# Kernel tuning notes

Measured on AMD Instinct MI355X. Metric: run time of the kernel, lower is better.

## Reference

```python
import jax, jax.numpy as jnp
import numpy as np

B, N, D, R, W, H, I = 256, 2048, 128, 4, 1, 1024, 1024
CI = I + R * D                       # controller input size (1536)
IF = 2 * D * W + 2 * W + 1 + 4 * R + D * R   # interface size (787)
OPI = H + R * D                      # output_proj input (1536)


def _norm(v):
    # F.normalize(dim=-1): x / max(||x||, eps)
    return v / jnp.maximum(jnp.linalg.norm(v, axis=-1, keepdims=True), 1e-12)


def setup_inputs() -> dict:
    key = jax.random.key(0)
    ks = jax.random.split(key, 16)
    u = lambda k, shape, fan: jax.random.uniform(k, shape, jnp.float32, -1.0 / np.sqrt(fan), 1.0 / np.sqrt(fan))
    return {
        "x": jax.random.normal(ks[0], (B, I), jnp.float32),
        "memory": jax.random.normal(ks[1], (N, D), jnp.float32) * np.sqrt(2.0 / (N + D)),  # xavier-ish
        "usage": jax.random.uniform(ks[2], (N,), jnp.float32),          # usage in [0,1)
        "link": jax.random.normal(ks[3], (N, N), jnp.float32) * 0.01,   # non-trivial link state
        "W_ih": u(ks[4], (4 * H, CI), H),
        "W_hh": u(ks[5], (4 * H, H), H),
        "b_ih": u(ks[6], (4 * H,), H),
        "b_hh": u(ks[7], (4 * H,), H),
        "W_if": u(ks[8], (IF, H), H),
        "b_if": u(ks[9], (IF,), H),
        "W_out": u(ks[10], (H, OPI), OPI),
        "b_out": u(ks[11], (H,), OPI),
    }


def reference(x, memory, usage, link, W_ih, W_hh, b_ih, b_hh, W_if, b_if, W_out, b_out):
    # initial uniform read weights (prev state at first step)
    prev_rw = jnp.full((B, R, N), 1.0 / N, x.dtype)
    read_flat = (prev_rw @ memory).reshape(B, -1)                 # (B, R*D)
    cin = jnp.concatenate([x, read_flat], axis=-1)                # (B, CI)

    # single LSTM step, h0 = c0 = 0, torch gate order i,f,g,o
    g = cin @ W_ih.T + b_ih + b_hh
    gi, gf, gg, go = jnp.split(g, 4, axis=-1)
    c = jax.nn.sigmoid(gi) * jnp.tanh(gg)
    h = jax.nn.sigmoid(go) * jnp.tanh(c)                          # (B, H) controller out

    itf = h @ W_if.T + b_if                                       # (B, IF)
    o = 0
    write_vals = itf[:, o:o + D * W].reshape(B, W, D); o += D * W
    erase = jax.nn.sigmoid(itf[:, o:o + D * W]).reshape(B, W, D); o += D * W
    write_gates = jax.nn.sigmoid(itf[:, o:o + W]); o += W         # (B, W)
    alloc_gate = jax.nn.sigmoid(itf[:, o:o + 1]); o += 1          # (B, 1)
    o += W                                                        # free gates (parsed, unused)
    read_modes = jax.nn.softmax(itf[:, o:o + 3 * R].reshape(B, R, 3), -1); o += 3 * R
    read_str = jax.nn.softplus(itf[:, o:o + R]); o += R           # (B, R)
    read_keys = itf[:, o:o + D * R].reshape(B, R, D)

    # content addressing for the write (strength = 1)
    mem_n = _norm(memory)
    cw = jax.nn.softmax(_norm(write_vals.mean(1)) @ mem_n.T, -1)  # (B, N)

    # allocation weighting: sorted-usage cumprod (per source semantics)
    idx = jnp.argsort(usage)
    su = usage[idx]
    cp = jnp.cumprod(1.0 - su)
    alloc_s = jnp.concatenate([su[:1], su[1:] * cp[:-1]])
    alloc = jnp.zeros_like(usage).at[idx].set(alloc_s)[None, :] * alloc_gate  # (B, N)

    write_w = write_gates[:, :, None] * (0.5 * cw + 0.5 * alloc)[:, None, :]  # (B, W, N)

    # temporal link update: batch-mean of diag-masked outer product, decay 0.9
    lu = jnp.einsum('bwn,bwm->nm', write_w, write_w) / B
    lu = lu * (1.0 - jnp.eye(N, dtype=lu.dtype))
    link_new = link * 0.9 + lu * 0.1

    # memory write (erase then add, batch-mean)
    ev = erase * write_gates[:, :, None]
    av = write_vals * write_gates[:, :, None]
    erase_mat = jnp.einsum('bwn,bwd->nd', write_w, ev) / B
    add_mat = jnp.einsum('bwn,bwd->nd', write_w, av) / B
    mem_new = memory * (1.0 - erase_mat) + add_mat

    # read addressing on updated memory and updated link (all R heads vectorized)
    sim = jnp.einsum('brd,nd->brn', _norm(read_keys), _norm(mem_new))
    content_r = jax.nn.softmax(sim * read_str[:, :, None], -1)    # (B, R, N)
    backward_w = jnp.einsum('brn,nm->brm', prev_rw, link_new)     # mode 1: prev @ L
    forward_w = jnp.einsum('brn,mn->brm', prev_rw, link_new)      # mode 2: prev @ L^T
    new_rw = (read_modes[..., 0:1] * content_r
              + read_modes[..., 1:2] * backward_w
              + read_modes[..., 2:3] * forward_w)                 # (B, R, N)

    read_out = (new_rw @ mem_new).reshape(B, -1)                  # (B, R*D)
    out = jnp.concatenate([h, read_out], axis=-1) @ W_out.T + b_out
    return out
```

## Files before the change

kernel.cpp:

```cpp
#include <hip/hip_runtime.h>
#include <cmath>

#define DEVI __device__ __forceinline__

DEVI float sigm(float x){ return 1.f/(1.f+expf(-x)); }

typedef __attribute__((ext_vector_type(8))) _Float16 half8;
typedef __attribute__((ext_vector_type(4))) _Float16 half4;
typedef __attribute__((ext_vector_type(4))) float float4v;


__global__ void k_zero(float* __restrict__ p, int n){
  int i = blockIdx.x*256 + threadIdx.x;
  if (i < n) p[i] = 0.f;
}

__global__ __launch_bounds__(256) void k_stage1(
    const float* __restrict__ mem, float* __restrict__ cm, _Float16* __restrict__ mem_h,
    const float* __restrict__ usage, float* __restrict__ alloc,
    const float* __restrict__ link, float* __restrict__ rsl, float* __restrict__ cslp)
{
  __shared__ float smem[4][132];
  const int blk = blockIdx.x, t = threadIdx.x;
  const int wv = t >> 6, lane = t & 63;

  if (blk < 128){
    int rbase = blk*16 + wv*4;
    float x0[4], x1[4], ss[4];
    #pragma unroll
    for (int u = 0; u < 4; u++){
      const float* a = mem + (size_t)(rbase+u)*128;
      x0[u] = a[lane]; x1[u] = a[lane+64];
    }
    #pragma unroll
    for (int u = 0; u < 4; u++) ss[u] = x0[u]*x0[u] + x1[u]*x1[u];
    #pragma unroll
    for (int o = 1; o < 64; o <<= 1){
      #pragma unroll
      for (int u = 0; u < 4; u++) ss[u] += __shfl_xor(ss[u], o);
    }
    float c0 = 0.f, c1 = 0.f;
    #pragma unroll
    for (int u = 0; u < 4; u++){
      float invn = 1.f / fmaxf(sqrtf(ss[u]), 1e-12f);
      mem_h[(size_t)(rbase+u)*128 + lane]      = (_Float16)(x0[u]*invn);
      mem_h[(size_t)(rbase+u)*128 + 64 + lane] = (_Float16)(x1[u]*invn);
      c0 += x0[u]; c1 += x1[u];
    }
    smem[wv][lane] = c0; smem[wv][64+lane] = c1;
    __syncthreads();
    if (t < 128) atomicAdd(&cm[t], smem[0][t]+smem[1][t]+smem[2][t]+smem[3][t]);
  } else if (blk < 384){
    int pb = blk - 128;
    int r0 = pb*8;
    int c0 = t*8;
    float4v v0[8], v1[8];
    #pragma unroll
    for (int u = 0; u < 8; u++){
      const float* lp = link + (size_t)(r0+u)*2048 + c0;
      v0[u] = *(const float4v*)lp;
      v1[u] = *(const float4v*)(lp+4);
    }
    float colacc[8];
    #pragma unroll
    for (int j = 0; j < 8; j++) colacc[j] = 0.f;
    float rowpart[8];
    #pragma unroll
    for (int u = 0; u < 8; u++){
      float s = 0.f;
      #pragma unroll
      for (int j = 0; j < 4; j++){
        colacc[j]   += v0[u][j]; colacc[4+j] += v1[u][j];
        s += v0[u][j] + v1[u][j];
      }
      rowpart[u] = s;
    }
    #pragma unroll
    for (int o = 1; o < 64; o <<= 1){
      #pragma unroll
      for (int u = 0; u < 8; u++) rowpart[u] += __shfl_xor(rowpart[u], o);
    }
    if (lane == 0){
      #pragma unroll
      for (int u = 0; u < 8; u++) smem[wv][u] = rowpart[u];
    }
    __syncthreads();
    if (t < 8) rsl[r0+t] = smem[0][t]+smem[1][t]+smem[2][t]+smem[3][t];
    float4v w0, w1;
    #pragma unroll
    for (int j = 0; j < 4; j++){ w0[j] = colacc[j]; w1[j] = colacc[4+j]; }
    *(float4v*)&cslp[(size_t)pb*2048 + c0]     = w0;
    *(float4v*)&cslp[(size_t)pb*2048 + c0 + 4] = w1;
  } else {
    int n = (blk - 384)*4 + wv;
    float un = usage[n];
    float prod = 1.f;
    #pragma unroll
    for (int i = 0; i < 32; i++){
      int m = lane + i*64;
      float um = usage[m];
      bool before = (um < un) || (um == un && m < n);
      prod *= before ? (1.f - um) : 1.f;
    }
    #pragma unroll
    for (int o = 32; o > 0; o >>= 1) prod *= __shfl_xor(prod, o);
    if (lane == 0) alloc[n] = un * prod;
  }
}

__global__ __launch_bounds__(256) void k_cin_csl(const float* __restrict__ x,
    const float* __restrict__ cm, _Float16* __restrict__ cin,
    const float* __restrict__ cslp, float* __restrict__ csl)
{
  __shared__ float sm[4][64];
  int blk = blockIdx.x, t = threadIdx.x;
  if (blk < 1536){
    int idx = blk*256 + t;
    int b = idx / 1536, k = idx - b*1536;
    float v = (k < 1024) ? x[b*1024 + k] : cm[(k-1024) & 127] * (1.f/2048.f);
    cin[idx] = (_Float16)v;
  } else {
    int j = blk - 1536;
    int tl = t & 63, q = t >> 6;
    int col = j*64 + tl;
    float s = 0.f;
    for (int p = q*64; p < q*64 + 64; p += 4){
      s += cslp[(size_t)(p+0)*2048 + col] + cslp[(size_t)(p+1)*2048 + col]
         + cslp[(size_t)(p+2)*2048 + col] + cslp[(size_t)(p+3)*2048 + col];
    }
    sm[q][tl] = s;
    __syncthreads();
    if (q == 0) csl[col] = sm[0][tl]+sm[1][tl]+sm[2][tl]+sm[3][tl];
  }
}

__global__ void k_lstm(const float* __restrict__ g, _Float16* __restrict__ h){
  int idx = blockIdx.x*256 + threadIdx.x;
  int b = idx >> 10, j = idx & 1023;
  const float* gr = g + (size_t)b*4096;
  float c = sigm(gr[j]) * tanhf(gr[2048 + j]);
  h[idx] = (_Float16)(sigm(gr[3072 + j]) * tanhf(c));
}

#define QA 264
#define QB 520

template<typename TB> struct BReg;
template<> struct BReg<_Float16>{
  half8 v;
  DEVI void load(const _Float16* p){ v = *(const half8*)p; }
  DEVI half8 get() const { return v; }
};
template<> struct BReg<float>{
  float4v a, b;
  DEVI void load(const float* p){ a = *(const float4v*)p; b = *(const float4v*)(p+4); }
  DEVI half8 get() const {
    half8 h;
    #pragma unroll
    for (int j = 0; j < 4; j++){ h[j] = (_Float16)a[j]; h[4+j] = (_Float16)b[j]; }
    return h;
  }
};

template<typename TB>
__global__ __launch_bounds__(256) void gemm_t(
    const _Float16* __restrict__ A, const TB* __restrict__ Bm, float* __restrict__ C,
    int M, int N, int K,
    const float* __restrict__ bias1, const float* __restrict__ bias2)
{
  __shared__ _Float16 Ah[2][8*QA];
  __shared__ _Float16 Bh[2][8*QB];
  const int tid = threadIdx.x;
  const int m0 = blockIdx.y*32, n0 = blockIdx.x*64;
  const int T = K >> 6;
  const int arow = tid >> 3, aq = tid & 7;
  const int brow = tid >> 3, bq = tid & 7;
  int nB0 = n0 + brow;      if (nB0 >= N) nB0 = N - 1;
  int nB1 = n0 + brow + 32; if (nB1 >= N) nB1 = N - 1;
  const _Float16* Aptr = A + (size_t)(m0 + arow)*K + aq*8;
  const TB* Bp0 = Bm + (size_t)nB0*K + bq*8;
  const TB* Bp1 = Bm + (size_t)nB1*K + bq*8;
  const int wA  = aq*QA + arow*8;
  const int wB0 = bq*QB + brow*8;
  const int wB1 = bq*QB + (brow+32)*8;
  const int wv_ = tid >> 6, lane = tid & 63;
  const int fq = lane >> 4, fr = lane & 15;
  const int m16 = (wv_ & 1)*16, nb = (wv_ >> 1)*32;

  half8 ra;
  BReg<TB> rb0, rb1;
  ra = *(const half8*)(Aptr);
  rb0.load(Bp0);
  rb1.load(Bp1);
  *(half8*)&Ah[0][wA]  = ra;
  *(half8*)&Bh[0][wB0] = rb0.get();
  *(half8*)&Bh[0][wB1] = rb1.get();
  __syncthreads();

  float4v acc0 = {0.f,0.f,0.f,0.f}, acc1 = {0.f,0.f,0.f,0.f};
  for (int t = 0; t < T; t++){
    const int cur = t & 1, nxt = cur ^ 1;
    if (t+1 < T){
      ra = *(const half8*)(Aptr + (t+1)*64);
      rb0.load(Bp0 + (t+1)*64);
      rb1.load(Bp1 + (t+1)*64);
    }
    #pragma unroll
    for (int s = 0; s < 2; s++){
      int q = s*4 + fq;
      half8 a  = *(half8*)&Ah[cur][q*QA + (m16+fr)*8];
      half8 b0 = *(half8*)&Bh[cur][q*QB + (nb+fr)*8];
      half8 b1 = *(half8*)&Bh[cur][q*QB + (nb+16+fr)*8];
      acc0 = __builtin_amdgcn_mfma_f32_16x16x32_f16(a, b0, acc0, 0, 0, 0);
      acc1 = __builtin_amdgcn_mfma_f32_16x16x32_f16(a, b1, acc1, 0, 0, 0);
    }
    if (t+1 < T){
      *(half8*)&Ah[nxt][wA]  = ra;
      *(half8*)&Bh[nxt][wB0] = rb0.get();
      *(half8*)&Bh[nxt][wB1] = rb1.get();
    }
    __syncthreads();
  }

  const int colA = n0 + nb + fr, colB = colA + 16;
  #pragma unroll
  for (int i = 0; i < 4; i++){
    int m = m0 + m16 + fq*4 + i;
    if (colA < N){
      float v = acc0[i];
      if (bias1) v += bias1[colA];
      if (bias2) v += bias2[colA];
      C[(size_t)m*N + colA] = v;
    }
    if (colB < N){
      float v = acc1[i];
      if (bias1) v += bias1[colB];
      if (bias2) v += bias2[colB];
      C[(size_t)m*N + colB] = v;
    }
  }
}

DEVI float blockReduce128(float v, float* lds2){
  #pragma unroll
  for (int o = 32; o > 0; o >>= 1) v += __shfl_xor(v, o);
  int w = threadIdx.x >> 6;
  __syncthreads();
  if ((threadIdx.x & 63) == 0) lds2[w] = v;
  __syncthreads();
  return lds2[0] + lds2[1];
}

__global__ __launch_bounds__(128) void k_parse(const float* __restrict__ itf,
    _Float16* __restrict__ wv_h, float* __restrict__ ev, float* __restrict__ av,
    float* __restrict__ wg_, float* __restrict__ ag_,
    float* __restrict__ rm0, float* __restrict__ rm1, float* __restrict__ rm2,
    _Float16* __restrict__ rks_h)
{
  __shared__ float red[2];
  int b = blockIdx.x, t = threadIdx.x;
  const float* it = itf + (size_t)b*787;
  float wg = sigm(it[256]);
  float ag = sigm(it[257]);
  if (t == 0){ wg_[b] = wg; ag_[b] = ag; }
  float w = it[t];
  av[b*128 + t] = w * wg;
  ev[b*128 + t] = sigm(it[128 + t]) * wg;
  float ss = blockReduce128(w*w, red);
  float invwv = 1.f / fmaxf(sqrtf(ss), 1e-12f);
  wv_h[b*128 + t] = (_Float16)(w * invwv);
  if (t < 4){
    int rr = t;
    float m0v = it[259 + rr*3 + 0], m1v = it[259 + rr*3 + 1], m2v = it[259 + rr*3 + 2];
    float mx = fmaxf(m0v, fmaxf(m1v, m2v));
    float e0 = expf(m0v - mx), e1 = expf(m1v - mx), e2 = expf(m2v - mx);
    float inv = 1.f / (e0 + e1 + e2);
    rm0[b*4 + rr] = e0*inv; rm1[b*4 + rr] = e1*inv; rm2[b*4 + rr] = e2*inv;
  }
  #pragma unroll
  for (int rr = 0; rr < 4; rr++){
    float kv = it[275 + rr*128 + t];
    float ks = blockReduce128(kv*kv, red);
    float sx = it[271 + rr];
    float str = fmaxf(sx, 0.f) + log1pf(expf(-fabsf(sx)));
    float invk = 1.f / fmaxf(sqrtf(ks), 1e-12f);
    rks_h[((size_t)b*4 + rr)*128 + t] = (_Float16)(kv * invk * str);
  }
}

__global__ __launch_bounds__(256) void k_softmax_ww(float* __restrict__ P,
    const float* __restrict__ alloc, const float* __restrict__ wg, const float* __restrict__ ag){
  __shared__ float red[4];
  float* p = P + (size_t)blockIdx.x*2048;
  int t = threadIdx.x;
  float r[8];
  float mx = -3.4e38f;
  #pragma unroll
  for (int i = 0; i < 8; i++){ r[i] = p[t + i*256]; mx = fmaxf(mx, r[i]); }
  #pragma unroll
  for (int o = 32; o > 0; o >>= 1) mx = fmaxf(mx, __shfl_xor(mx, o));
  if ((t & 63) == 0) red[t >> 6] = mx;
  __syncthreads();
  mx = fmaxf(fmaxf(red[0], red[1]), fmaxf(red[2], red[3]));
  float s = 0.f;
  #pragma unroll
  for (int i = 0; i < 8; i++){ r[i] = expf(r[i] - mx); s += r[i]; }
  #pragma unroll
  for (int o = 32; o > 0; o >>= 1) s += __shfl_xor(s, o);
  __syncthreads();
  if ((t & 63) == 0) red[t >> 6] = s;
  __syncthreads();
  s = red[0] + red[1] + red[2] + red[3];
  float inv = 1.f / s;
  float wgb = wg[blockIdx.x], agb = ag[blockIdx.x];
  #pragma unroll
  for (int i = 0; i < 8; i++){
    int col = t + i*256;
    p[col] = wgb*(0.5f*r[i]*inv + 0.5f*alloc[col]*agb);
  }
}

__global__ __launch_bounds__(256) void k_bwfw(const float* __restrict__ ww,
                       const float* __restrict__ wg, const float* __restrict__ ag,
                       const float* __restrict__ alloc,
                       const float* __restrict__ rowsum, const float* __restrict__ colsum,
                       float* __restrict__ bw, float* __restrict__ fw){
  __shared__ float sq[4][64], sd[4][64];
  __shared__ float sred[4];
  __shared__ float tbs[256];
  int t = threadIdx.x & 63, z = threadIdx.x >> 6;
  int m = blockIdx.x*64 + t;
  float sa = 0.f;
  #pragma unroll
  for (int i = 0; i < 8; i++) sa += alloc[threadIdx.x + i*256];
  #pragma unroll
  for (int o = 32; o > 0; o >>= 1) sa += __shfl_xor(sa, o);
  if (t == 0) sred[z] = sa;
  __syncthreads();
  sa = (sred[0]+sred[1]) + (sred[2]+sred[3]);
  tbs[threadIdx.x] = wg[threadIdx.x]*(0.5f + 0.5f*ag[threadIdx.x]*sa);
  __syncthreads();
  float q = 0.f, dd = 0.f;
  for (int b = z*64; b < z*64 + 64; b += 4){
    float w0 = ww[(size_t)(b+0)*2048 + m];
    float w1 = ww[(size_t)(b+1)*2048 + m];
    float w2 = ww[(size_t)(b+2)*2048 + m];
    float w3 = ww[(size_t)(b+3)*2048 + m];
    q  = fmaf(tbs[b+0], w0, q);  dd = fmaf(w0, w0, dd);
    q  = fmaf(tbs[b+1], w1, q);  dd = fmaf(w1, w1, dd);
    q  = fmaf(tbs[b+2], w2, q);  dd = fmaf(w2, w2, dd);
    q  = fmaf(tbs[b+3], w3, q);  dd = fmaf(w3, w3, dd);
  }
  sq[z][t] = q; sd[z][t] = dd;
  __syncthreads();
  if (z == 0){
    q  = sq[0][t] + sq[1][t] + sq[2][t] + sq[3][t];
    dd = sd[0][t] + sd[1][t] + sd[2][t] + sd[3][t];
    float lus = (q - dd) * (1.f/256.f);
    bw[m] = (0.9f*colsum[m] + 0.1f*lus) * (1.f/2048.f);
    fw[m] = (0.9f*rowsum[m] + 0.1f*lus) * (1.f/2048.f);
  }
}

__global__ __launch_bounds__(256) void k_memupdate_fused(const float* __restrict__ ww,
    const float* __restrict__ ev, const float* __restrict__ av,
    const float* __restrict__ mem, const float* __restrict__ bw, const float* __restrict__ fw,
    _Float16* __restrict__ memn_h, _Float16* __restrict__ memnT_h,
    float* __restrict__ bwm, float* __restrict__ fwm)
{
  __shared__ float Ws[16][34];
  __shared__ float Es[16][132], Vs[16][132];
  __shared__ float lb[128], lf[128];
  __shared__ _Float16 Traw[32][132];
  const int n0 = blockIdx.x*32;
  const int tid = threadIdx.x, tx = tid & 31, ty = tid >> 5;
  if (tid < 128){ lb[tid] = 0.f; lf[tid] = 0.f; }
  const int wk = tid >> 4, wn = (tid & 15)*2;
  const int ek = tid >> 4, ec = (tid & 15)*8;
  float ae[4][4] = {}, aa[4][4] = {};
  for (int k0 = 0; k0 < 256; k0 += 16){
    float2 vw  = *(const float2*)(ww + (size_t)(k0+wk)*2048 + n0 + wn);
    float4 ve0 = *(const float4*)(ev + (size_t)(k0+ek)*128 + ec);
    float4 ve1 = *(const float4*)(ev + (size_t)(k0+ek)*128 + ec + 4);
    float4 va0 = *(const float4*)(av + (size_t)(k0+ek)*128 + ec);
    float4 va1 = *(const float4*)(av + (size_t)(k0+ek)*128 + ec + 4);
    __syncthreads();
    Ws[wk][wn] = vw.x; Ws[wk][wn+1] = vw.y;
    *(float4*)&Es[ek][ec] = ve0; *(float4*)&Es[ek][ec+4] = ve1;
    *(float4*)&Vs[ek][ec] = va0; *(float4*)&Vs[ek][ec+4] = va1;
    __syncthreads();
    #pragma unroll
    for (int k = 0; k < 16; k++){
      float a[4], e[4], v[4];
      #pragma unroll
      for (int i = 0; i < 4; i++) a[i] = Ws[k][ty*4+i];
      #pragma unroll
      for (int j = 0; j < 4; j++){ e[j] = Es[k][tx*4+j]; v[j] = Vs[k][tx*4+j]; }
      #pragma unroll
      for (int i = 0; i < 4; i++)
        #pragma unroll
        for (int j = 0; j < 4; j++){
          ae[i][j] = fmaf(a[i], e[j], ae[i][j]);
          aa[i][j] = fmaf(a[i], v[j], aa[i][j]);
        }
    }
  }
  float ab[4] = {0,0,0,0}, af[4] = {0,0,0,0};
  #pragma unroll
  for (int i = 0; i < 4; i++){
    int n = n0 + ty*4 + i;
    float bwn = bw[n], fwn = fw[n];
    float v[4]; float ss = 0.f;
    #pragma unroll
    for (int j = 0; j < 4; j++){
      int d = tx*4 + j;
      float em = ae[i][j]*(1.f/256.f), am = aa[i][j]*(1.f/256.f);
      float mv = mem[(size_t)n*128 + d]*(1.f - em) + am;
      v[j] = mv; ss += mv*mv;
      ab[j] = fmaf(bwn, mv, ab[j]);
      af[j] = fmaf(fwn, mv, af[j]);
    }
    #pragma unroll
    for (int o = 1; o < 32; o <<= 1) ss += __shfl_xor(ss, o);
    float invn = 1.f / fmaxf(sqrtf(ss), 1e-12f);
    half4 hn, hr;
    #pragma unroll
    for (int j = 0; j < 4; j++){ hn[j] = (_Float16)(v[j]*invn); hr[j] = (_Float16)v[j]; }
    *(half4*)(memn_h + (size_t)n*128 + tx*4) = hn;
    *(half4*)&Traw[ty*4+i][tx*4] = hr;
  }
  __syncthreads();
  {
    int d = tid >> 1, seg = (tid & 1)*16;
    half8 o0, o1;
    #pragma unroll
    for (int j = 0; j < 8; j++){ o0[j] = Traw[seg+j][d]; o1[j] = Traw[seg+8+j][d]; }
    *(half8*)(memnT_h + (size_t)d*2048 + n0 + seg)     = o0;
    *(half8*)(memnT_h + (size_t)d*2048 + n0 + seg + 8) = o1;
  }
  #pragma unroll
  for (int j = 0; j < 4; j++){
    atomicAdd(&lb[tx*4+j], ab[j]);
    atomicAdd(&lf[tx*4+j], af[j]);
  }
  __syncthreads();
  if (tid < 128){
    atomicAdd(&bwm[tid], lb[tid]);
    atomicAdd(&fwm[tid], lf[tid]);
  }
}

__global__ __launch_bounds__(256) void k_flash(
    const _Float16* __restrict__ Q, const _Float16* __restrict__ Kh,
    const _Float16* __restrict__ Vt,
    float* __restrict__ pacc, float* __restrict__ pm, float* __restrict__ pl)
{
  __shared__ _Float16 Pl[4][16][32];
  __shared__ float cmb[4][2080];
  __shared__ float scl[4][16];
  const int tid = threadIdx.x;
  const int qt = blockIdx.x >> 2, kc = blockIdx.x & 3;
  const int wv = tid >> 6, lane = tid & 63;
  const int fq = lane >> 4, fr = lane & 15;
  const int kw0 = kc*512 + wv*128;

  half8 aq[4];
  #pragma unroll
  for (int c = 0; c < 4; c++)
    aq[c] = *(const half8*)(Q + (size_t)(qt*16 + fr)*128 + c*32 + fq*8);

  float m[4] = {-3.0e38f,-3.0e38f,-3.0e38f,-3.0e38f};
  float l[4] = {0.f,0.f,0.f,0.f};
  float4v acc[8] = {};
  for (int s = 0; s < 4; s++){
    const int kb = kw0 + s*32;
    float4v S0 = {0,0,0,0}, S1 = {0,0,0,0};
    #pragma unroll
    for (int c = 0; c < 4; c++){
      half8 b0 = *(const half8*)(Kh + (size_t)(kb + fr)*128      + c*32 + fq*8);
      half8 b1 = *(const half8*)(Kh + (size_t)(kb + 16 + fr)*128 + c*32 + fq*8);
      S0 = __builtin_amdgcn_mfma_f32_16x16x32_f16(aq[c], b0, S0, 0, 0, 0);
      S1 = __builtin_amdgcn_mfma_f32_16x16x32_f16(aq[c], b1, S1, 0, 0, 0);
    }
    float mt[4], ps[4];
    #pragma unroll
    for (int i = 0; i < 4; i++) mt[i] = fmaxf(S0[i], S1[i]);
    #pragma unroll
    for (int o = 1; o < 16; o <<= 1){
      #pragma unroll
      for (int i = 0; i < 4; i++) mt[i] = fmaxf(mt[i], __shfl_xor(mt[i], o));
    }
    #pragma unroll
    for (int i = 0; i < 4; i++){
      float mn = fmaxf(m[i], mt[i]);
      float al = expf(m[i] - mn);
      float p0 = expf(S0[i] - mn), p1 = expf(S1[i] - mn);
      S0[i] = p0; S1[i] = p1;
      ps[i] = p0 + p1;
      l[i] *= al;
      m[i] = mn;
      #pragma unroll
      for (int c = 0; c < 8; c++) acc[c][i] *= al;
    }
    #pragma unroll
    for (int o = 1; o < 16; o <<= 1){
      #pragma unroll
      for (int i = 0; i < 4; i++) ps[i] += __shfl_xor(ps[i], o);
    }
    #pragma unroll
    for (int i = 0; i < 4; i++) l[i] += ps[i];
    #pragma unroll
    for (int i = 0; i < 4; i++){
      Pl[wv][fq*4+i][fr]      = (_Float16)S0[i];
      Pl[wv][fq*4+i][16 + fr] = (_Float16)S1[i];
    }
    half8 pf = *(half8*)&Pl[wv][fr][fq*8];
    #pragma unroll
    for (int c = 0; c < 8; c++){
      half8 bv = *(const half8*)(Vt + (size_t)(c*16 + fr)*2048 + kb + fq*8);
      acc[c] = __builtin_amdgcn_mfma_f32_16x16x32_f16(pf, bv, acc[c], 0, 0, 0);
    }
  }
  if (fr == 0){
    #pragma unroll
    for (int i = 0; i < 4; i++){
      cmb[wv][fq*4+i]      = m[i];
      cmb[wv][16 + fq*4+i] = l[i];
    }
  }
  #pragma unroll
  for (int c = 0; c < 8; c++)
    #pragma unroll
    for (int i = 0; i < 4; i++)
      cmb[wv][32 + (fq*4+i)*128 + c*16 + fr] = acc[c][i];
  __syncthreads();
  if (tid < 16){
    float mm = fmaxf(fmaxf(cmb[0][tid], cmb[1][tid]), fmaxf(cmb[2][tid], cmb[3][tid]));
    float ll = 0.f;
    #pragma unroll
    for (int w = 0; w < 4; w++){
      float e = expf(cmb[w][tid] - mm);
      scl[w][tid] = e;
      ll += e * cmb[w][16 + tid];
    }
    pm[blockIdx.x*16 + tid] = mm;
    pl[blockIdx.x*16 + tid] = ll;
  }
  __syncthreads();
  for (int e = tid; e < 2048; e += 256){
    int q = e >> 7;
    float a = scl[0][q]*cmb[0][32+e] + scl[1][q]*cmb[1][32+e]
            + scl[2][q]*cmb[2][32+e] + scl[3][q]*cmb[3][32+e];
    pacc[(size_t)blockIdx.x*2048 + e] = a;
  }
}

__global__ void k_hro_comb(const _Float16* __restrict__ h, const float* __restrict__ pacc,
                           const float* __restrict__ pm, const float* __restrict__ pl,
                           const float* __restrict__ rm0, const float* __restrict__ rm1,
                           const float* __restrict__ rm2, const float* __restrict__ bwm,
                           const float* __restrict__ fwm, _Float16* __restrict__ hro){
  int idx = blockIdx.x*256 + threadIdx.x;
  int b = idx / 1536, k = idx - b*1536;
  if (k < 1024){
    hro[idx] = h[b*1024 + k];
  } else {
    int r = k - 1024, rh = r >> 7, d = r & 127;
    int row = b*4 + rh, qt = row >> 4, q = row & 15;
    float mm = -3.0e38f;
    #pragma unroll
    for (int kc = 0; kc < 4; kc++) mm = fmaxf(mm, pm[(qt*4+kc)*16 + q]);
    float num = 0.f, den = 0.f;
    #pragma unroll
    for (int kc = 0; kc < 4; kc++){
      float e = expf(pm[(qt*4+kc)*16 + q] - mm);
      den += e * pl[(qt*4+kc)*16 + q];
      num += e * pacc[(size_t)(qt*4+kc)*2048 + q*128 + d];
    }
    float pv = num / den;
    hro[idx] = (_Float16)(rm0[row]*pv + rm1[row]*bwm[d] + rm2[row]*fwm[d]);
  }
}


extern "C" void kernel_launch(void* const* d_in, const int* in_sizes, int n_in,
                              void* d_out, int out_size, void* d_ws, size_t ws_size,
                              hipStream_t stream)
{
  const float* x     = (const float*)d_in[0];
  const float* mem   = (const float*)d_in[1];
  const float* usage = (const float*)d_in[2];
  const float* link  = (const float*)d_in[3];
  const float* W_ih  = (const float*)d_in[4];
  const float* b_ih  = (const float*)d_in[6];
  const float* b_hh  = (const float*)d_in[7];
  const float* W_if  = (const float*)d_in[8];
  const float* b_if  = (const float*)d_in[9];
  const float* W_out = (const float*)d_in[10];
  const float* b_out = (const float*)d_in[11];
  float* out = (float*)d_out;
  float* ws  = (float*)d_ws;

  float* cm     = ws + 0;
  float* csl    = ws + 128;
  float* bwm    = ws + 2176;
  float* fwm    = ws + 2304;
  float* bw     = ws + 2688;
  float* fw     = ws + 4736;
  float* wg     = ws + 6784;
  float* ag     = ws + 7040;
  float* rm0    = ws + 7296;
  float* rm1    = ws + 8320;
  float* rm2    = ws + 9344;
  float* alloc  = ws + 10368;
  float* rsl    = ws + 12416;
  float* ev     = ws + 14464;
  float* av     = ws + 47232;
  float* g      = ws + 80000;
  float* itf    = ws + 1128576;
  float* ww     = ws + 1330048;
  float* pacc   = ws + 1854336;
  float* pm     = ws + 2378624;
  float* pl     = ws + 2382720;
  _Float16* wv_h    = (_Float16*)(ws + 2386816);
  _Float16* mem_h   = (_Float16*)(ws + 2403200);
  _Float16* memn_h  = (_Float16*)(ws + 2534272);
  _Float16* memnT_h = (_Float16*)(ws + 2665344);
  _Float16* rks_h   = (_Float16*)(ws + 2796416);
  _Float16* hro_h   = (_Float16*)(ws + 2861952);
  _Float16* cin_h   = (_Float16*)(ws + 3058560);
  _Float16* h_h     = (_Float16*)(ws + 3255168);
  float* cslp       = ws + 3386240;

  k_zero<<<10, 256, 0, stream>>>(ws, 2432);

  k_stage1<<<896, 256, 0, stream>>>(mem, cm, mem_h, usage, alloc, link, rsl, cslp);
  k_cin_csl<<<1568, 256, 0, stream>>>(x, cm, cin_h, cslp, csl);

  gemm_t<float><<<dim3(64,8), 256, 0, stream>>>(cin_h, W_ih, g, 256, 4096, 1536, b_ih, b_hh);
  k_lstm<<<1024, 256, 0, stream>>>(g, h_h);

  gemm_t<float><<<dim3(13,8), 256, 0, stream>>>(h_h, W_if, itf, 256, 787, 1024, b_if, nullptr);
  k_parse<<<256, 128, 0, stream>>>(itf, wv_h, ev, av, wg, ag, rm0, rm1, rm2, rks_h);

  gemm_t<_Float16><<<dim3(32,8), 256, 0, stream>>>(wv_h, mem_h, ww, 256, 2048, 128, nullptr, nullptr);
  k_softmax_ww<<<256, 256, 0, stream>>>(ww, alloc, wg, ag);

  k_bwfw<<<32, 256, 0, stream>>>(ww, wg, ag, alloc, rsl, csl, bw, fw);

  k_memupdate_fused<<<64, 256, 0, stream>>>(ww, ev, av, mem, bw, fw, memn_h, memnT_h, bwm, fwm);

  k_flash<<<256, 256, 0, stream>>>(rks_h, memn_h, memnT_h, pacc, pm, pl);

  k_hro_comb<<<1536, 256, 0, stream>>>(h_h, pacc, pm, pl, rm0, rm1, rm2, bwm, fwm, hro_h);
  gemm_t<float><<<dim3(16,8), 256, 0, stream>>>(hro_h, W_out, out, 256, 1024, 1536, b_out, nullptr);

  (void)in_sizes; (void)n_in; (void)out_size; (void)ws_size;
}
```

Baseline: 236.3 us.

## Fuse LSTM gates into W_ih GEMM, skip forget gate, fold bwfw into memupdate

A dedicated GEMM kernel computes only the input, cell and output gate columns of W_ih. The forget gate is unused because c0 is zero, so this skips a quarter of that GEMM. The kernel applies the LSTM nonlinearity in its epilogue, which removes the fp32 gate buffer round-trip and the separate k_lstm launch. The k_bwfw reduction over write weights is also folded into k_memupdate_fused, reusing the ww tiles already staged in shared memory and dropping one launch plus the bw/fw global buffers. The trade-off is more registers and LDS in both kernels, and a smaller 32x32 output tile in the LSTM GEMM.

```diff
diff --git a/kernel.cpp b/kernel.cpp
--- a/kernel.cpp
+++ b/kernel.cpp
@@ -134,16 +134,9 @@
   }
 }
 
-__global__ void k_lstm(const float* __restrict__ g, _Float16* __restrict__ h){
-  int idx = blockIdx.x*256 + threadIdx.x;
-  int b = idx >> 10, j = idx & 1023;
-  const float* gr = g + (size_t)b*4096;
-  float c = sigm(gr[j]) * tanhf(gr[2048 + j]);
-  h[idx] = (_Float16)(sigm(gr[3072 + j]) * tanhf(c));
-}
-
 #define QA 264
 #define QB 520
+#define QB3 776
 
 template<typename TB> struct BReg;
 template<> struct BReg<_Float16>{
@@ -238,6 +231,96 @@
       if (bias2) v += bias2[colB];
       C[(size_t)m*N + colB] = v;
     }
+  }
+}
+
+__global__ __launch_bounds__(256) void k_gemm_lstm(
+    const _Float16* __restrict__ A, const float* __restrict__ W,
+    const float* __restrict__ b_ih, const float* __restrict__ b_hh,
+    _Float16* __restrict__ h)
+{
+  __shared__ _Float16 Ah[2][8*QA];
+  __shared__ _Float16 Bh[2][8*QB3];
+  const int tid = threadIdx.x;
+  const int m0 = blockIdx.y*32, c0 = blockIdx.x*32;
+  const int T = 24;
+  const int arow = tid >> 3, aq = tid & 7;
+  const int brow = tid >> 3, bq = tid & 7;
+  const _Float16* Aptr = A + (size_t)(m0 + arow)*1536 + aq*8;
+  const float* Bpi = W + (size_t)(       c0 + brow)*1536 + bq*8;
+  const float* Bpg = W + (size_t)(2048 + c0 + brow)*1536 + bq*8;
+  const float* Bpo = W + (size_t)(3072 + c0 + brow)*1536 + bq*8;
+  const int wA  = aq*QA + arow*8;
+  const int wBi = bq*QB3 + brow*8;
+  const int wBg = bq*QB3 + (32+brow)*8;
+  const int wBo = bq*QB3 + (64+brow)*8;
+  const int wv_ = tid >> 6, lane = tid & 63;
+  const int fq = lane >> 4, fr = lane & 15;
+  const int m16 = (wv_ & 1)*16, c16 = (wv_ >> 1)*16;
+
+  half8 ra0, ra1;
+  BReg<float> ri0, rg0, ro0, ri1, rg1, ro1;
+  ra0 = *(const half8*)(Aptr);
+  ri0.load(Bpi); rg0.load(Bpg); ro0.load(Bpo);
+  ra1 = *(const half8*)(Aptr + 64);
+  ri1.load(Bpi + 64); rg1.load(Bpg + 64); ro1.load(Bpo + 64);
+  *(half8*)&Ah[0][wA]  = ra0;
+  *(half8*)&Bh[0][wBi] = ri0.get();
+  *(half8*)&Bh[0][wBg] = rg0.get();
+  *(half8*)&Bh[0][wBo] = ro0.get();
+  __syncthreads();
+
+  float4v acci = {0.f,0.f,0.f,0.f}, accg = {0.f,0.f,0.f,0.f}, acco = {0.f,0.f,0.f,0.f};
+  for (int t = 0; t < T; t++){
+    const int cur = t & 1, nxt = cur ^ 1;
+    if (t+2 < T){
+      if (cur == 0){
+        ra0 = *(const half8*)(Aptr + (t+2)*64);
+        ri0.load(Bpi + (t+2)*64); rg0.load(Bpg + (t+2)*64); ro0.load(Bpo + (t+2)*64);
+      } else {
+        ra1 = *(const half8*)(Aptr + (t+2)*64);
+        ri1.load(Bpi + (t+2)*64); rg1.load(Bpg + (t+2)*64); ro1.load(Bpo + (t+2)*64);
+      }
+    }
+    #pragma unroll
+    for (int s = 0; s < 2; s++){
+      int q = s*4 + fq;
+      half8 a  = *(half8*)&Ah[cur][q*QA + (m16+fr)*8];
+      half8 bi = *(half8*)&Bh[cur][q*QB3 + (c16+fr)*8];
+      half8 bg = *(half8*)&Bh[cur][q*QB3 + (32+c16+fr)*8];
+      half8 bo = *(half8*)&Bh[cur][q*QB3 + (64+c16+fr)*8];
+      acci = __builtin_amdgcn_mfma_f32_16x16x32_f16(a, bi, acci, 0, 0, 0);
+      accg = __builtin_amdgcn_mfma_f32_16x16x32_f16(a, bg, accg, 0, 0, 0);
+      acco = __builtin_amdgcn_mfma_f32_16x16x32_f16(a, bo, acco, 0, 0, 0);
+    }
+    if (t+1 < T){
+      if (nxt == 1){
+        *(half8*)&Ah[1][wA]  = ra1;
+        *(half8*)&Bh[1][wBi] = ri1.get();
+        *(half8*)&Bh[1][wBg] = rg1.get();
+        *(half8*)&Bh[1][wBo] = ro1.get();
+      } else {
+        *(half8*)&Ah[0][wA]  = ra0;
+        *(half8*)&Bh[0][wBi] = ri0.get();
+        *(half8*)&Bh[0][wBg] = rg0.get();
+        *(half8*)&Bh[0][wBo] = ro0.get();
+      }
+    }
+    __syncthreads();
+  }
+
+  const int col = c0 + c16 + fr;
+  const float bi1 = b_ih[col]        + b_hh[col];
+  const float bg1 = b_ih[2048 + col] + b_hh[2048 + col];
+  const float bo1 = b_ih[3072 + col] + b_hh[3072 + col];
+  #pragma unroll
+  for (int i = 0; i < 4; i++){
+    int m = m0 + m16 + fq*4 + i;
+    float gi = acci[i] + bi1;
+    float gg = accg[i] + bg1;
+    float go = acco[i] + bo1;
+    float c = sigm(gi) * tanhf(gg);
+    h[(size_t)m*1024 + col] = (_Float16)(sigm(go) * tanhf(c));
   }
 }
 
@@ -320,51 +403,12 @@
   }
 }
 
-__global__ __launch_bounds__(256) void k_bwfw(const float* __restrict__ ww,
-                       const float* __restrict__ wg, const float* __restrict__ ag,
-                       const float* __restrict__ alloc,
-                       const float* __restrict__ rowsum, const float* __restrict__ colsum,
-                       float* __restrict__ bw, float* __restrict__ fw){
-  __shared__ float sq[4][64], sd[4][64];
-  __shared__ float sred[4];
-  __shared__ float tbs[256];
-  int t = threadIdx.x & 63, z = threadIdx.x >> 6;
-  int m = blockIdx.x*64 + t;
-  float sa = 0.f;
-  #pragma unroll
-  for (int i = 0; i < 8; i++) sa += alloc[threadIdx.x + i*256];
-  #pragma unroll
-  for (int o = 32; o > 0; o >>= 1) sa += __shfl_xor(sa, o);
-  if (t == 0) sred[z] = sa;
-  __syncthreads();
-  sa = (sred[0]+sred[1]) + (sred[2]+sred[3]);
-  tbs[threadIdx.x] = wg[threadIdx.x]*(0.5f + 0.5f*ag[threadIdx.x]*sa);
-  __syncthreads();
-  float q = 0.f, dd = 0.f;
-  for (int b = z*64; b < z*64 + 64; b += 4){
-    float w0 = ww[(size_t)(b+0)*2048 + m];
-    float w1 = ww[(size_t)(b+1)*2048 + m];
-    float w2 = ww[(size_t)(b+2)*2048 + m];
-    float w3 = ww[(size_t)(b+3)*2048 + m];
-    q  = fmaf(tbs[b+0], w0, q);  dd = fmaf(w0, w0, dd);
-    q  = fmaf(tbs[b+1], w1, q);  dd = fmaf(w1, w1, dd);
-    q  = fmaf(tbs[b+2], w2, q);  dd = fmaf(w2, w2, dd);
-    q  = fmaf(tbs[b+3], w3, q);  dd = fmaf(w3, w3, dd);
-  }
-  sq[z][t] = q; sd[z][t] = dd;
-  __syncthreads();
-  if (z == 0){
-    q  = sq[0][t] + sq[1][t] + sq[2][t] + sq[3][t];
-    dd = sd[0][t] + sd[1][t] + sd[2][t] + sd[3][t];
-    float lus = (q - dd) * (1.f/256.f);
-    bw[m] = (0.9f*colsum[m] + 0.1f*lus) * (1.f/2048.f);
-    fw[m] = (0.9f*rowsum[m] + 0.1f*lus) * (1.f/2048.f);
-  }
-}
-
 __global__ __launch_bounds__(256) void k_memupdate_fused(const float* __restrict__ ww,
     const float* __restrict__ ev, const float* __restrict__ av,
-    const float* __restrict__ mem, const float* __restrict__ bw, const float* __restrict__ fw,
+    const float* __restrict__ mem,
+    const float* __restrict__ wg, const float* __restrict__ ag,
+    const float* __restrict__ alloc,
+    const float* __restrict__ rsl, const float* __restrict__ csl,
     _Float16* __restrict__ memn_h, _Float16* __restrict__ memnT_h,
     float* __restrict__ bwm, float* __restrict__ fwm)
 {
@@ -372,12 +416,30 @@
   __shared__ float Es[16][132], Vs[16][132];
   __shared__ float lb[128], lf[128];
   __shared__ _Float16 Traw[32][132];
+  __shared__ float tbs[256];
+  __shared__ float sq[8][32], sd[8][32];
+  __shared__ float bwL[32], fwL[32];
+  __shared__ float sred[4];
   const int n0 = blockIdx.x*32;
   const int tid = threadIdx.x, tx = tid & 31, ty = tid >> 5;
-  if (tid < 128){ lb[tid] = 0.f; lf[tid] = 0.f; }
+
+  {
+    float sa = 0.f;
+    #pragma unroll
+    for (int i = 0; i < 8; i++) sa += alloc[tid + i*256];
+    #pragma unroll
+    for (int o = 32; o > 0; o >>= 1) sa += __shfl_xor(sa, o);
+    if ((tid & 63) == 0) sred[tid >> 6] = sa;
+    if (tid < 128){ lb[tid] = 0.f; lf[tid] = 0.f; }
+    __syncthreads();
+    sa = (sred[0]+sred[1]) + (sred[2]+sred[3]);
+    tbs[tid] = wg[tid]*(0.5f + 0.5f*ag[tid]*sa);
+  }
+
   const int wk = tid >> 4, wn = (tid & 15)*2;
   const int ek = tid >> 4, ec = (tid & 15)*8;
   float ae[4][4] = {}, aa[4][4] = {};
+  float qp = 0.f, ddp = 0.f;
   for (int k0 = 0; k0 < 256; k0 += 16){
     float2 vw  = *(const float2*)(ww + (size_t)(k0+wk)*2048 + n0 + wn);
     float4 ve0 = *(const float4*)(ev + (size_t)(k0+ek)*128 + ec);
@@ -404,12 +466,29 @@
           aa[i][j] = fmaf(a[i], v[j], aa[i][j]);
         }
     }
-  }
+    {
+      float w0 = Ws[ty*2+0][tx], w1 = Ws[ty*2+1][tx];
+      qp  = fmaf(tbs[k0+ty*2+0], w0, qp);  ddp = fmaf(w0, w0, ddp);
+      qp  = fmaf(tbs[k0+ty*2+1], w1, qp);  ddp = fmaf(w1, w1, ddp);
+    }
+  }
+  sq[ty][tx] = qp; sd[ty][tx] = ddp;
+  __syncthreads();
+  if (tid < 32){
+    float q = 0.f, dd = 0.f;
+    #pragma unroll
+    for (int z = 0; z < 8; z++){ q += sq[z][tid]; dd += sd[z][tid]; }
+    float lus = (q - dd) * (1.f/256.f);
+    bwL[tid] = (0.9f*csl[n0+tid] + 0.1f*lus) * (1.f/2048.f);
+    fwL[tid] = (0.9f*rsl[n0+tid] + 0.1f*lus) * (1.f/2048.f);
+  }
+  __syncthreads();
+
   float ab[4] = {0,0,0,0}, af[4] = {0,0,0,0};
   #pragma unroll
   for (int i = 0; i < 4; i++){
     int n = n0 + ty*4 + i;
-    float bwn = bw[n], fwn = fw[n];
+    float bwn = bwL[ty*4+i], fwn = fwL[ty*4+i];
     float v[4]; float ss = 0.f;
     #pragma unroll
     for (int j = 0; j < 4; j++){
@@ -605,8 +684,6 @@
   float* csl    = ws + 128;
   float* bwm    = ws + 2176;
   float* fwm    = ws + 2304;
-  float* bw     = ws + 2688;
-  float* fw     = ws + 4736;
   float* wg     = ws + 6784;
   float* ag     = ws + 7040;
   float* rm0    = ws + 7296;
@@ -616,7 +693,6 @@
   float* rsl    = ws + 12416;
   float* ev     = ws + 14464;
   float* av     = ws + 47232;
-  float* g      = ws + 80000;
   float* itf    = ws + 1128576;
   float* ww     = ws + 1330048;
   float* pacc   = ws + 1854336;
@@ -637,8 +713,7 @@
   k_stage1<<<896, 256, 0, stream>>>(mem, cm, mem_h, usage, alloc, link, rsl, cslp);
   k_cin_csl<<<1568, 256, 0, stream>>>(x, cm, cin_h, cslp, csl);
 
-  gemm_t<float><<<dim3(64,8), 256, 0, stream>>>(cin_h, W_ih, g, 256, 4096, 1536, b_ih, b_hh);
-  k_lstm<<<1024, 256, 0, stream>>>(g, h_h);
+  k_gemm_lstm<<<dim3(32,8), 256, 0, stream>>>(cin_h, W_ih, b_ih, b_hh, h_h);
 
   gemm_t<float><<<dim3(13,8), 256, 0, stream>>>(h_h, W_if, itf, 256, 787, 1024, b_if, nullptr);
   k_parse<<<256, 128, 0, stream>>>(itf, wv_h, ev, av, wg, ag, rm0, rm1, rm2, rks_h);
@@ -646,9 +721,8 @@
   gemm_t<_Float16><<<dim3(32,8), 256, 0, stream>>>(wv_h, mem_h, ww, 256, 2048, 128, nullptr, nullptr);
   k_softmax_ww<<<256, 256, 0, stream>>>(ww, alloc, wg, ag);
 
-  k_bwfw<<<32, 256, 0, stream>>>(ww, wg, ag, alloc, rsl, csl, bw, fw);
-
-  k_memupdate_fused<<<64, 256, 0, stream>>>(ww, ev, av, mem, bw, fw, memn_h, memnT_h, bwm, fwm);
+  k_memupdate_fused<<<64, 256, 0, stream>>>(ww, ev, av, mem, wg, ag, alloc, rsl, csl,
+                                            memn_h, memnT_h, bwm, fwm);
 
   k_flash<<<256, 256, 0, stream>>>(rks_h, memn_h, memnT_h, pacc, pm, pl);
 
```

Measured after the change: 238.1 us. Within noise of the previous version (+0.8%).
